# Kernel optimization log

Hardware: AMD Instinct MI355X
Metric: run time of the kernel (lower is better)

The kernel has to match this reference:

```python
import jax, jax.numpy as jnp
import numpy as np

DIST_THRESH = 2.5


def _level_losses(lvl_cls, lvl_reg, gt_boxes, gt_labels):
    # lvl_cls: [B, HW, nc], lvl_reg: [B, HW, 4], gt_boxes: [B, N, 4], gt_labels: [B, N]
    gt_xy = gt_boxes[..., :2]            # [B, N, 2]
    pred_xy = lvl_reg[..., :2]           # [B, HW, 2]
    # squared euclidean distances [B, N, HW] (cdist equivalent; min/argmin unaffected by sqrt)
    d2 = jnp.sum((gt_xy[:, :, None, :] - pred_xy[:, None, :, :]) ** 2, axis=-1)
    min_d2 = jnp.min(d2, axis=2)         # [B, N]
    matches = jnp.argmin(d2, axis=2)     # [B, N]
    valid = jnp.sqrt(min_d2) < DIST_THRESH  # [B, N] bool
    # gather matched predictions per gt
    g_cls = jnp.take_along_axis(lvl_cls, matches[..., None], axis=1)   # [B, N, nc]
    g_reg = jnp.take_along_axis(lvl_reg, matches[..., None], axis=1)   # [B, N, 4]
    # cross entropy (reduction='none'), summed over valid matches
    logp = jax.nn.log_softmax(g_cls, axis=-1)
    ce = -jnp.take_along_axis(logp, gt_labels[..., None], axis=-1)[..., 0]  # [B, N]
    l1 = jnp.abs(g_reg - gt_boxes).sum(axis=-1)                             # [B, N]
    w = valid.astype(lvl_cls.dtype)
    return (ce * w).sum(), (l1 * w).sum(), w.sum()


def setup_inputs() -> dict:
    key = jax.random.key(0)
    ks = jax.random.split(key, 8)
    B, N, nc = 16, 128, 80
    hws = [25600, 6400, 1600]
    inp = {}
    for i, hw in enumerate(hws):
        inp[f"pred_cls_{i}"] = jax.random.normal(ks[i], (B, hw, nc), dtype=jnp.float32)
        inp[f"pred_reg_{i}"] = jax.random.normal(ks[3 + i], (B, hw, 4), dtype=jnp.float32)
    inp["gt_boxes"] = jax.random.normal(ks[6], (B, N, 4), dtype=jnp.float32)
    inp["gt_labels"] = jax.random.randint(ks[7], (B, N), 0, nc)
    return inp


def reference(pred_cls_0, pred_cls_1, pred_cls_2,
              pred_reg_0, pred_reg_1, pred_reg_2,
              gt_boxes, gt_labels):
    cls_list = [pred_cls_0, pred_cls_1, pred_cls_2]
    reg_list = [pred_reg_0, pred_reg_1, pred_reg_2]
    cls_loss = jnp.zeros((), jnp.float32)
    reg_loss = jnp.zeros((), jnp.float32)
    num_pos = jnp.zeros((), jnp.float32)
    for lvl_cls, lvl_reg in zip(cls_list, reg_list):
        c, r, n = _level_losses(lvl_cls, lvl_reg, gt_boxes, gt_labels)
        cls_loss = cls_loss + c
        reg_loss = reg_loss + r
        num_pos = num_pos + n
    denom = jnp.maximum(num_pos, 1.0)
    return cls_loss / denom, reg_loss / denom, num_pos
```

## Files before the change

### kernel.cpp

```cpp
#include <hip/hip_runtime.h>
#include <cstdint>
#include <cstddef>

#define NTH 256
#define NGT 128
#define BATCH 16
#define NC 80
#define G 16
#define NCHUNK (NGT / G)
#define HW0 25600
#define HW1 6400
#define HW2 1600
#define SL0 4
#define MAXSL 4
#define NLOSS_BLK (3 * BATCH * NGT / 4)

#define PACK0_OFF 0
#define PACK1_OFF (PACK0_OFF + BATCH * HW0 * 8)
#define PACK2_OFF (PACK1_OFF + BATCH * HW1 * 8)
#define PART_OFF  (PACK2_OFF + BATCH * HW2 * 8)
#define PART_BYTES (3 * BATCH * NGT * MAXSL * 8)
#define PARTL_OFF (PART_OFF + PART_BYTES)
#define PARTL_BYTES (NLOSS_BLK * 3 * sizeof(float))
#define WS_NEEDED (PARTL_OFF + (size_t)PARTL_BYTES)

__device__ __forceinline__ unsigned long long umin64(unsigned long long a, unsigned long long b) {
    return a < b ? a : b;
}

__global__ __launch_bounds__(NTH) void pack_kernel(
    const float* __restrict__ reg0, const float* __restrict__ reg1, const float* __restrict__ reg2,
    float2* __restrict__ xy0, float2* __restrict__ xy1, float2* __restrict__ xy2)
{
    int r = blockIdx.x * NTH + threadIdx.x;
    const int N0 = BATCH * HW0, N1 = BATCH * HW1, N2 = BATCH * HW2;
    if (r < N0) {
        float4 v = reinterpret_cast<const float4*>(reg0)[r];
        xy0[r] = make_float2(v.x, v.y);
    } else if (r < N0 + N1) {
        int i = r - N0;
        float4 v = reinterpret_cast<const float4*>(reg1)[i];
        xy1[i] = make_float2(v.x, v.y);
    } else if (r < N0 + N1 + N2) {
        int i = r - N0 - N1;
        float4 v = reinterpret_cast<const float4*>(reg2)[i];
        xy2[i] = make_float2(v.x, v.y);
    }
}

#define EVAL(px, py, idx_) do {                                                   \
    _Pragma("unroll")                                                             \
    for (int g = 0; g < G; ++g) {                                                 \
        float dx = gx[g] - (px), dy = gy[g] - (py);                               \
        float d2 = dx * dx + dy * dy;                                             \
        unsigned long long key =                                                  \
            ((unsigned long long)__float_as_uint(d2) << 32) | (unsigned)(idx_);   \
        kmin[g] = umin64(kmin[g], key);                                           \
    } } while (0)

__global__ __launch_bounds__(NTH) void scan_kernel(
    const float2* __restrict__ xy0, const float2* __restrict__ xy1, const float2* __restrict__ xy2,
    int stride2,
    const float* __restrict__ gt_boxes,
    unsigned long long* __restrict__ part)
{
    int x = blockIdx.x;
    int lvl, b, slice, chunk, HW, nsl;
    const float2* src;
    if (x < BATCH * SL0 * NCHUNK) {
        lvl = 0; b = x / (SL0 * NCHUNK);
        int r = x % (SL0 * NCHUNK);
        slice = r / NCHUNK; chunk = r % NCHUNK;
        HW = HW0; nsl = SL0; src = xy0;
    } else if (x < BATCH * SL0 * NCHUNK + BATCH * NCHUNK) {
        int y = x - BATCH * SL0 * NCHUNK;
        lvl = 1; b = y / NCHUNK; chunk = y % NCHUNK; slice = 0;
        HW = HW1; nsl = 1; src = xy1;
    } else {
        int y = x - BATCH * SL0 * NCHUNK - BATCH * NCHUNK;
        lvl = 2; b = y / NCHUNK; chunk = y % NCHUNK; slice = 0;
        HW = HW2; nsl = 1; src = xy2;
    }

    const int seg = HW / nsl;
    const int e0 = slice * seg, e1 = e0 + seg;
    const int tid = threadIdx.x, wave = tid >> 6, lane = tid & 63;
    const int n0 = chunk * G;

    float gx[G], gy[G];
#pragma unroll
    for (int g = 0; g < G; ++g) {
        const float* gb = gt_boxes + (size_t)(b * NGT + n0 + g) * 4;
        gx[g] = gb[0]; gy[g] = gb[1];
    }

    unsigned long long kmin[G];
#pragma unroll
    for (int g = 0; g < G; ++g) kmin[g] = ~0ull;

    if (stride2 == 1) {
        const float4* b4 = reinterpret_cast<const float4*>(src + (size_t)b * HW);
        for (int i = e0 / 2 + tid; i < e1 / 2; i += NTH) {
            float4 p = b4[i];
            int i0 = 2 * i;
            EVAL(p.x, p.y, i0);
            EVAL(p.z, p.w, i0 + 1);
        }
    } else {
        const float2* base = src + (size_t)b * HW * 2;
        for (int i = e0 + tid; i < e1; i += NTH) {
            float2 p = base[(size_t)i * 2];
            EVAL(p.x, p.y, i);
        }
    }

#pragma unroll
    for (int g = 0; g < G; ++g) {
#pragma unroll
        for (int off = 32; off >= 1; off >>= 1) {
            unsigned long long o = __shfl_down(kmin[g], off, 64);
            kmin[g] = umin64(kmin[g], o);
        }
    }

    __shared__ unsigned long long smem[G][4];
    if (lane == 0) {
#pragma unroll
        for (int g = 0; g < G; ++g) smem[g][wave] = kmin[g];
    }
    __syncthreads();

    if (tid < G) {
        unsigned long long key = umin64(umin64(smem[tid][0], smem[tid][1]),
                                        umin64(smem[tid][2], smem[tid][3]));
        part[((size_t)(lvl * BATCH + b) * NGT + n0 + tid) * MAXSL + slice] = key;
    }
}

__global__ __launch_bounds__(NTH) void loss_kernel(
    const float* __restrict__ cls0, const float* __restrict__ cls1, const float* __restrict__ cls2,
    const float* __restrict__ reg0, const float* __restrict__ reg1, const float* __restrict__ reg2,
    const float* __restrict__ gt_boxes, const int* __restrict__ gt_labels,
    const unsigned long long* __restrict__ part, float* __restrict__ partl)
{
    const int wave = threadIdx.x >> 6;
    const int lane = threadIdx.x & 63;
    const int gid = blockIdx.x * 4 + wave;
    const int lvl = gid / (BATCH * NGT);
    const int r = gid % (BATCH * NGT);
    const int b = r / NGT, n = r % NGT;

    const float* cls; const float* reg; int HW, S;
    if (lvl == 0)      { cls = cls0; reg = reg0; HW = HW0; S = SL0; }
    else if (lvl == 1) { cls = cls1; reg = reg1; HW = HW1; S = 1; }
    else               { cls = cls2; reg = reg2; HW = HW2; S = 1; }

    const unsigned long long* p = part + (size_t)gid * MAXSL;
    unsigned long long key = p[0];
    for (int s = 1; s < S; ++s) key = umin64(key, p[s]);

    int match = (int)(unsigned)(key & 0xffffffffu);
    float d2min = __uint_as_float((unsigned)(key >> 32));
    bool valid = d2min < 6.25f;

    const int label = gt_labels[b * NGT + n];
    const float* c = cls + ((size_t)b * HW + match) * NC;

    float x1 = c[lane];
    float x2 = (lane < NC - 64) ? c[64 + lane] : -INFINITY;
    float mx = fmaxf(x1, x2);
#pragma unroll
    for (int off = 32; off >= 1; off >>= 1) mx = fmaxf(mx, __shfl_xor(mx, off, 64));
    float s = expf(x1 - mx) + ((lane < NC - 64) ? expf(x2 - mx) : 0.0f);
#pragma unroll
    for (int off = 32; off >= 1; off >>= 1) s += __shfl_xor(s, off, 64);

    __shared__ float ce_s[4], l1_s[4], w_s[4];
    if (lane == 0) {
        float ce = 0.0f, l1 = 0.0f, w = 0.0f;
        if (valid) {
            float xlab = c[label];
            ce = -(xlab - mx - logf(s));
            const float* gb = gt_boxes + (size_t)(b * NGT + n) * 4;
            const float* gr = reg + ((size_t)b * HW + match) * 4;
            l1 = fabsf(gr[0] - gb[0]) + fabsf(gr[1] - gb[1]) +
                 fabsf(gr[2] - gb[2]) + fabsf(gr[3] - gb[3]);
            w = 1.0f;
        }
        ce_s[wave] = ce; l1_s[wave] = l1; w_s[wave] = w;
    }
    __syncthreads();

    if (threadIdx.x == 0) {
        float* o = partl + (size_t)blockIdx.x * 3;
        o[0] = ce_s[0] + ce_s[1] + ce_s[2] + ce_s[3];
        o[1] = l1_s[0] + l1_s[1] + l1_s[2] + l1_s[3];
        o[2] = w_s[0] + w_s[1] + w_s[2] + w_s[3];
    }
}

__global__ __launch_bounds__(NTH) void finalize_kernel(
    const float* __restrict__ partl, float* __restrict__ out)
{
    const int tid = threadIdx.x, wave = tid >> 6, lane = tid & 63;
    float ce = 0.0f, l1 = 0.0f, w = 0.0f;
    for (int i = tid; i < NLOSS_BLK; i += NTH) {
        ce += partl[(size_t)i * 3 + 0];
        l1 += partl[(size_t)i * 3 + 1];
        w  += partl[(size_t)i * 3 + 2];
    }
#pragma unroll
    for (int off = 32; off >= 1; off >>= 1) {
        ce += __shfl_xor(ce, off, 64);
        l1 += __shfl_xor(l1, off, 64);
        w  += __shfl_xor(w,  off, 64);
    }
    __shared__ float sm[3][4];
    if (lane == 0) { sm[0][wave] = ce; sm[1][wave] = l1; sm[2][wave] = w; }
    __syncthreads();
    if (tid == 0) {
        float tce = sm[0][0] + sm[0][1] + sm[0][2] + sm[0][3];
        float tl1 = sm[1][0] + sm[1][1] + sm[1][2] + sm[1][3];
        float tw  = sm[2][0] + sm[2][1] + sm[2][2] + sm[2][3];
        float denom = fmaxf(tw, 1.0f);
        out[0] = tce / denom;
        out[1] = tl1 / denom;
        out[2] = tw;
    }
}

extern "C" void kernel_launch(void* const* d_in, const int* in_sizes, int n_in,
                              void* d_out, int out_size, void* d_ws, size_t ws_size,
                              hipStream_t stream) {
    const float* cls0 = nullptr; const float* cls1 = nullptr; const float* cls2 = nullptr;
    const float* reg0 = nullptr; const float* reg1 = nullptr; const float* reg2 = nullptr;
    const float* gt_boxes = nullptr; const int* gt_labels = nullptr;
    for (int i = 0; i < n_in; ++i) {
        switch (in_sizes[i]) {
            case BATCH * HW0 * NC: cls0 = (const float*)d_in[i]; break;
            case BATCH * HW1 * NC: cls1 = (const float*)d_in[i]; break;
            case BATCH * HW2 * NC: cls2 = (const float*)d_in[i]; break;
            case BATCH * HW0 * 4:  reg0 = (const float*)d_in[i]; break;
            case BATCH * HW1 * 4:  reg1 = (const float*)d_in[i]; break;
            case BATCH * HW2 * 4:  reg2 = (const float*)d_in[i]; break;
            case BATCH * NGT * 4:  gt_boxes = (const float*)d_in[i]; break;
            case BATCH * NGT:      gt_labels = (const int*)d_in[i]; break;
            default: break;
        }
    }

    char* ws = (char*)d_ws;
    const bool pack = (ws_size >= WS_NEEDED);
    unsigned long long* part;
    float* partl;
    const int scan_grid = BATCH * SL0 * NCHUNK + 2 * BATCH * NCHUNK;

    if (pack) {
        float2* xy0 = (float2*)(ws + PACK0_OFF);
        float2* xy1 = (float2*)(ws + PACK1_OFF);
        float2* xy2 = (float2*)(ws + PACK2_OFF);
        part  = (unsigned long long*)(ws + PART_OFF);
        partl = (float*)(ws + PARTL_OFF);
        const int rows = BATCH * (HW0 + HW1 + HW2);
        pack_kernel<<<(rows + NTH - 1) / NTH, NTH, 0, stream>>>(
            reg0, reg1, reg2, xy0, xy1, xy2);
        scan_kernel<<<scan_grid, NTH, 0, stream>>>(
            xy0, xy1, xy2, 1, gt_boxes, part);
    } else {
        part  = (unsigned long long*)(ws);
        partl = (float*)(ws + PART_BYTES);
        scan_kernel<<<scan_grid, NTH, 0, stream>>>(
            (const float2*)reg0, (const float2*)reg1, (const float2*)reg2, 2,
            gt_boxes, part);
    }

    loss_kernel<<<NLOSS_BLK, NTH, 0, stream>>>(
        cls0, cls1, cls2, reg0, reg1, reg2, gt_boxes, gt_labels, part, partl);

    finalize_kernel<<<1, NTH, 0, stream>>>(partl, (float*)d_out);
}
```

Before: 221.4 us.

## Fuse scan, loss and finalize into one kernel with atomic last-block reductions

```diff
diff --git a/kernel.cpp b/kernel.cpp
--- a/kernel.cpp
+++ b/kernel.cpp
@@ -12,40 +12,28 @@
 #define HW1 6400
 #define HW2 1600
 #define SL0 4
-#define MAXSL 4
-#define NLOSS_BLK (3 * BATCH * NGT / 4)
-
-#define PACK0_OFF 0
-#define PACK1_OFF (PACK0_OFF + BATCH * HW0 * 8)
-#define PACK2_OFF (PACK1_OFF + BATCH * HW1 * 8)
-#define PART_OFF  (PACK2_OFF + BATCH * HW2 * 8)
-#define PART_BYTES (3 * BATCH * NGT * MAXSL * 8)
-#define PARTL_OFF (PART_OFF + PART_BYTES)
-#define PARTL_BYTES (NLOSS_BLK * 3 * sizeof(float))
-#define WS_NEEDED (PARTL_OFF + (size_t)PARTL_BYTES)
+
+#define NGRP0 (BATCH * NCHUNK)
+#define GRID0 (BATCH * SL0 * NCHUNK)
+#define GRID1 (BATCH * NCHUNK)
+#define GRID2 (BATCH * NCHUNK)
+#define GRID  (GRID0 + GRID1 + GRID2)
+#define NLOSS (3 * NGRP0)
+
+#define PART_OFF   0
+#define PART_BYTES (NGRP0 * G * SL0 * 8)
+#define PARTL_OFF  PART_BYTES
+#define PARTL_BYTES (NLOSS * 3 * 4)
+#define CTR_OFF    (PARTL_OFF + PARTL_BYTES)
+#define NCTR       (NGRP0 + 1)
+#define WS_NEEDED  ((size_t)CTR_OFF + (size_t)NCTR * 4)
 
 __device__ __forceinline__ unsigned long long umin64(unsigned long long a, unsigned long long b) {
     return a < b ? a : b;
 }
 
-__global__ __launch_bounds__(NTH) void pack_kernel(
-    const float* __restrict__ reg0, const float* __restrict__ reg1, const float* __restrict__ reg2,
-    float2* __restrict__ xy0, float2* __restrict__ xy1, float2* __restrict__ xy2)
-{
-    int r = blockIdx.x * NTH + threadIdx.x;
-    const int N0 = BATCH * HW0, N1 = BATCH * HW1, N2 = BATCH * HW2;
-    if (r < N0) {
-        float4 v = reinterpret_cast<const float4*>(reg0)[r];
-        xy0[r] = make_float2(v.x, v.y);
-    } else if (r < N0 + N1) {
-        int i = r - N0;
-        float4 v = reinterpret_cast<const float4*>(reg1)[i];
-        xy1[i] = make_float2(v.x, v.y);
-    } else if (r < N0 + N1 + N2) {
-        int i = r - N0 - N1;
-        float4 v = reinterpret_cast<const float4*>(reg2)[i];
-        xy2[i] = make_float2(v.x, v.y);
-    }
+__global__ __launch_bounds__(NTH) void zero_kernel(unsigned int* __restrict__ ctrs) {
+    if (threadIdx.x < NCTR) ctrs[threadIdx.x] = 0u;
 }
 
 #define EVAL(px, py, idx_) do {                                                   \
@@ -58,28 +46,37 @@
         kmin[g] = umin64(kmin[g], key);                                           \
     } } while (0)
 
-__global__ __launch_bounds__(NTH) void scan_kernel(
-    const float2* __restrict__ xy0, const float2* __restrict__ xy1, const float2* __restrict__ xy2,
-    int stride2,
-    const float* __restrict__ gt_boxes,
-    unsigned long long* __restrict__ part)
+__global__ __launch_bounds__(NTH) void fused_kernel(
+    const float* __restrict__ cls0, const float* __restrict__ cls1, const float* __restrict__ cls2,
+    const float* __restrict__ reg0, const float* __restrict__ reg1, const float* __restrict__ reg2,
+    const float* __restrict__ gt_boxes, const int* __restrict__ gt_labels,
+    unsigned long long* __restrict__ part, float* __restrict__ partl,
+    unsigned int* __restrict__ ctrs, float* __restrict__ out)
 {
-    int x = blockIdx.x;
+    __shared__ unsigned long long red[G][4];
+    __shared__ unsigned long long keyS[G];
+    __shared__ float tr[3][4];
+    __shared__ float fm[3][4];
+    __shared__ int flag;
+    __shared__ int lastG;
+
+    const int x = blockIdx.x;
     int lvl, b, slice, chunk, HW, nsl;
-    const float2* src;
-    if (x < BATCH * SL0 * NCHUNK) {
+    const float* reg;
+    const float* cls;
+    if (x < GRID0) {
         lvl = 0; b = x / (SL0 * NCHUNK);
         int r = x % (SL0 * NCHUNK);
         slice = r / NCHUNK; chunk = r % NCHUNK;
-        HW = HW0; nsl = SL0; src = xy0;
-    } else if (x < BATCH * SL0 * NCHUNK + BATCH * NCHUNK) {
-        int y = x - BATCH * SL0 * NCHUNK;
+        HW = HW0; nsl = SL0; reg = reg0; cls = cls0;
+    } else if (x < GRID0 + GRID1) {
+        int y = x - GRID0;
         lvl = 1; b = y / NCHUNK; chunk = y % NCHUNK; slice = 0;
-        HW = HW1; nsl = 1; src = xy1;
+        HW = HW1; nsl = 1; reg = reg1; cls = cls1;
     } else {
-        int y = x - BATCH * SL0 * NCHUNK - BATCH * NCHUNK;
+        int y = x - GRID0 - GRID1;
         lvl = 2; b = y / NCHUNK; chunk = y % NCHUNK; slice = 0;
-        HW = HW2; nsl = 1; src = xy2;
+        HW = HW2; nsl = 1; reg = reg2; cls = cls2;
     }
 
     const int seg = HW / nsl;
@@ -98,20 +95,10 @@
 #pragma unroll
     for (int g = 0; g < G; ++g) kmin[g] = ~0ull;
 
-    if (stride2 == 1) {
-        const float4* b4 = reinterpret_cast<const float4*>(src + (size_t)b * HW);
-        for (int i = e0 / 2 + tid; i < e1 / 2; i += NTH) {
-            float4 p = b4[i];
-            int i0 = 2 * i;
-            EVAL(p.x, p.y, i0);
-            EVAL(p.z, p.w, i0 + 1);
-        }
-    } else {
-        const float2* base = src + (size_t)b * HW * 2;
-        for (int i = e0 + tid; i < e1; i += NTH) {
-            float2 p = base[(size_t)i * 2];
-            EVAL(p.x, p.y, i);
-        }
+    const float4* rows = reinterpret_cast<const float4*>(reg) + (size_t)b * HW;
+    for (int i = e0 + tid; i < e1; i += NTH) {
+        float4 p = rows[i];
+        EVAL(p.x, p.y, i);
     }
 
 #pragma unroll
@@ -122,92 +109,89 @@
             kmin[g] = umin64(kmin[g], o);
         }
     }
-
-    __shared__ unsigned long long smem[G][4];
     if (lane == 0) {
 #pragma unroll
-        for (int g = 0; g < G; ++g) smem[g][wave] = kmin[g];
-    }
-    __syncthreads();
-
-    if (tid < G) {
-        unsigned long long key = umin64(umin64(smem[tid][0], smem[tid][1]),
-                                        umin64(smem[tid][2], smem[tid][3]));
-        part[((size_t)(lvl * BATCH + b) * NGT + n0 + tid) * MAXSL + slice] = key;
-    }
-}
-
-__global__ __launch_bounds__(NTH) void loss_kernel(
-    const float* __restrict__ cls0, const float* __restrict__ cls1, const float* __restrict__ cls2,
-    const float* __restrict__ reg0, const float* __restrict__ reg1, const float* __restrict__ reg2,
-    const float* __restrict__ gt_boxes, const int* __restrict__ gt_labels,
-    const unsigned long long* __restrict__ part, float* __restrict__ partl)
-{
-    const int wave = threadIdx.x >> 6;
-    const int lane = threadIdx.x & 63;
-    const int gid = blockIdx.x * 4 + wave;
-    const int lvl = gid / (BATCH * NGT);
-    const int r = gid % (BATCH * NGT);
-    const int b = r / NGT, n = r % NGT;
-
-    const float* cls; const float* reg; int HW, S;
-    if (lvl == 0)      { cls = cls0; reg = reg0; HW = HW0; S = SL0; }
-    else if (lvl == 1) { cls = cls1; reg = reg1; HW = HW1; S = 1; }
-    else               { cls = cls2; reg = reg2; HW = HW2; S = 1; }
-
-    const unsigned long long* p = part + (size_t)gid * MAXSL;
-    unsigned long long key = p[0];
-    for (int s = 1; s < S; ++s) key = umin64(key, p[s]);
-
-    int match = (int)(unsigned)(key & 0xffffffffu);
-    float d2min = __uint_as_float((unsigned)(key >> 32));
-    bool valid = d2min < 6.25f;
-
-    const int label = gt_labels[b * NGT + n];
-    const float* c = cls + ((size_t)b * HW + match) * NC;
-
-    float x1 = c[lane];
-    float x2 = (lane < NC - 64) ? c[64 + lane] : -INFINITY;
-    float mx = fmaxf(x1, x2);
-#pragma unroll
-    for (int off = 32; off >= 1; off >>= 1) mx = fmaxf(mx, __shfl_xor(mx, off, 64));
-    float s = expf(x1 - mx) + ((lane < NC - 64) ? expf(x2 - mx) : 0.0f);
-#pragma unroll
-    for (int off = 32; off >= 1; off >>= 1) s += __shfl_xor(s, off, 64);
-
-    __shared__ float ce_s[4], l1_s[4], w_s[4];
-    if (lane == 0) {
-        float ce = 0.0f, l1 = 0.0f, w = 0.0f;
-        if (valid) {
-            float xlab = c[label];
-            ce = -(xlab - mx - logf(s));
-            const float* gb = gt_boxes + (size_t)(b * NGT + n) * 4;
-            const float* gr = reg + ((size_t)b * HW + match) * 4;
-            l1 = fabsf(gr[0] - gb[0]) + fabsf(gr[1] - gb[1]) +
-                 fabsf(gr[2] - gb[2]) + fabsf(gr[3] - gb[3]);
-            w = 1.0f;
-        }
-        ce_s[wave] = ce; l1_s[wave] = l1; w_s[wave] = w;
-    }
-    __syncthreads();
-
-    if (threadIdx.x == 0) {
-        float* o = partl + (size_t)blockIdx.x * 3;
-        o[0] = ce_s[0] + ce_s[1] + ce_s[2] + ce_s[3];
-        o[1] = l1_s[0] + l1_s[1] + l1_s[2] + l1_s[3];
-        o[2] = w_s[0] + w_s[1] + w_s[2] + w_s[3];
-    }
-}
-
-__global__ __launch_bounds__(NTH) void finalize_kernel(
-    const float* __restrict__ partl, float* __restrict__ out)
-{
-    const int tid = threadIdx.x, wave = tid >> 6, lane = tid & 63;
+        for (int g = 0; g < G; ++g) red[g][wave] = kmin[g];
+    }
+    __syncthreads();
+
+    const int wslot = lvl * NGRP0 + b * NCHUNK + chunk;
+
+    if (lvl == 0) {
+        const int grp = b * NCHUNK + chunk;
+        if (tid < G) {
+            unsigned long long kfin = umin64(umin64(red[tid][0], red[tid][1]),
+                                             umin64(red[tid][2], red[tid][3]));
+            part[((size_t)grp * G + tid) * SL0 + slice] = kfin;
+            __threadfence();
+        }
+        __syncthreads();
+        if (tid == 0) flag = (atomicAdd(&ctrs[grp], 1u) == SL0 - 1) ? 1 : 0;
+        __syncthreads();
+        if (!flag) return;
+        __threadfence();
+        if (tid < G) {
+            const unsigned long long* p = part + ((size_t)grp * G + tid) * SL0;
+            keyS[tid] = umin64(umin64(p[0], p[1]), umin64(p[2], p[3]));
+        }
+        __syncthreads();
+    } else {
+        if (tid < G) {
+            keyS[tid] = umin64(umin64(red[tid][0], red[tid][1]),
+                               umin64(red[tid][2], red[tid][3]));
+        }
+        __syncthreads();
+    }
+
+    float ceA = 0.0f, l1A = 0.0f, wA = 0.0f;
+#pragma unroll
+    for (int sub = 0; sub < 4; ++sub) {
+        const int nl = wave * 4 + sub;
+        const unsigned long long key = keyS[nl];
+        const float d2min = __uint_as_float((unsigned)(key >> 32));
+        if (d2min < 6.25f) {
+            const int match = (int)(unsigned)(key & 0xffffffffu);
+            const int n = n0 + nl;
+            const float* c = cls + ((size_t)b * HW + match) * NC;
+            float x1 = c[lane];
+            float x2 = (lane < NC - 64) ? c[64 + lane] : -INFINITY;
+            float mx = fmaxf(x1, x2);
+#pragma unroll
+            for (int off = 32; off >= 1; off >>= 1) mx = fmaxf(mx, __shfl_xor(mx, off, 64));
+            float sden = expf(x1 - mx) + ((lane < NC - 64) ? expf(x2 - mx) : 0.0f);
+#pragma unroll
+            for (int off = 32; off >= 1; off >>= 1) sden += __shfl_xor(sden, off, 64);
+            if (lane == 0) {
+                const int label = gt_labels[b * NGT + n];
+                const float xlab = c[label];
+                ceA += -(xlab - mx - logf(sden));
+                const float* gb = gt_boxes + (size_t)(b * NGT + n) * 4;
+                const float* gr = reg + ((size_t)b * HW + match) * 4;
+                l1A += fabsf(gr[0] - gb[0]) + fabsf(gr[1] - gb[1]) +
+                       fabsf(gr[2] - gb[2]) + fabsf(gr[3] - gb[3]);
+                wA += 1.0f;
+            }
+        }
+    }
+
+    if (lane == 0) { tr[0][wave] = ceA; tr[1][wave] = l1A; tr[2][wave] = wA; }
+    __syncthreads();
+    if (tid == 0) {
+        float* o = partl + (size_t)wslot * 3;
+        o[0] = tr[0][0] + tr[0][1] + tr[0][2] + tr[0][3];
+        o[1] = tr[1][0] + tr[1][1] + tr[1][2] + tr[1][3];
+        o[2] = tr[2][0] + tr[2][1] + tr[2][2] + tr[2][3];
+        __threadfence();
+        lastG = (atomicAdd(&ctrs[NGRP0], 1u) == NLOSS - 1) ? 1 : 0;
+    }
+    __syncthreads();
+    if (!lastG) return;
+
+    __threadfence();
     float ce = 0.0f, l1 = 0.0f, w = 0.0f;
-    for (int i = tid; i < NLOSS_BLK; i += NTH) {
-        ce += partl[(size_t)i * 3 + 0];
-        l1 += partl[(size_t)i * 3 + 1];
-        w  += partl[(size_t)i * 3 + 2];
+    for (int i = tid; i < NLOSS; i += NTH) {
+        const float* o = partl + (size_t)i * 3;
+        ce += o[0]; l1 += o[1]; w += o[2];
     }
 #pragma unroll
     for (int off = 32; off >= 1; off >>= 1) {
@@ -215,13 +199,12 @@
         l1 += __shfl_xor(l1, off, 64);
         w  += __shfl_xor(w,  off, 64);
     }
-    __shared__ float sm[3][4];
-    if (lane == 0) { sm[0][wave] = ce; sm[1][wave] = l1; sm[2][wave] = w; }
+    if (lane == 0) { fm[0][wave] = ce; fm[1][wave] = l1; fm[2][wave] = w; }
     __syncthreads();
     if (tid == 0) {
-        float tce = sm[0][0] + sm[0][1] + sm[0][2] + sm[0][3];
-        float tl1 = sm[1][0] + sm[1][1] + sm[1][2] + sm[1][3];
-        float tw  = sm[2][0] + sm[2][1] + sm[2][2] + sm[2][3];
+        float tce = fm[0][0] + fm[0][1] + fm[0][2] + fm[0][3];
+        float tl1 = fm[1][0] + fm[1][1] + fm[1][2] + fm[1][3];
+        float tw  = fm[2][0] + fm[2][1] + fm[2][2] + fm[2][3];
         float denom = fmaxf(tw, 1.0f);
         out[0] = tce / denom;
         out[1] = tl1 / denom;
@@ -250,32 +233,12 @@
     }
 
     char* ws = (char*)d_ws;
-    const bool pack = (ws_size >= WS_NEEDED);
-    unsigned long long* part;
-    float* partl;
-    const int scan_grid = BATCH * SL0 * NCHUNK + 2 * BATCH * NCHUNK;
-
-    if (pack) {
-        float2* xy0 = (float2*)(ws + PACK0_OFF);
-        float2* xy1 = (float2*)(ws + PACK1_OFF);
-        float2* xy2 = (float2*)(ws + PACK2_OFF);
-        part  = (unsigned long long*)(ws + PART_OFF);
-        partl = (float*)(ws + PARTL_OFF);
-        const int rows = BATCH * (HW0 + HW1 + HW2);
-        pack_kernel<<<(rows + NTH - 1) / NTH, NTH, 0, stream>>>(
-            reg0, reg1, reg2, xy0, xy1, xy2);
-        scan_kernel<<<scan_grid, NTH, 0, stream>>>(
-            xy0, xy1, xy2, 1, gt_boxes, part);
-    } else {
-        part  = (unsigned long long*)(ws);
-        partl = (float*)(ws + PART_BYTES);
-        scan_kernel<<<scan_grid, NTH, 0, stream>>>(
-            (const float2*)reg0, (const float2*)reg1, (const float2*)reg2, 2,
-            gt_boxes, part);
-    }
-
-    loss_kernel<<<NLOSS_BLK, NTH, 0, stream>>>(
-        cls0, cls1, cls2, reg0, reg1, reg2, gt_boxes, gt_labels, part, partl);
-
-    finalize_kernel<<<1, NTH, 0, stream>>>(partl, (float*)d_out);
-}
+    unsigned long long* part = (unsigned long long*)(ws + PART_OFF);
+    float* partl             = (float*)(ws + PARTL_OFF);
+    unsigned int* ctrs       = (unsigned int*)(ws + CTR_OFF);
+
+    zero_kernel<<<1, NTH, 0, stream>>>(ctrs);
+    fused_kernel<<<GRID, NTH, 0, stream>>>(
+        cls0, cls1, cls2, reg0, reg1, reg2, gt_boxes, gt_labels,
+        part, partl, ctrs, (float*)d_out);
+}
```

Measured after the change: 251.0 us. 1.13x slower.
